# Kernel tuning notes

Hardware: AMD Instinct MI355X
Metric: run time of the kernel (lower is better)

Reference implementation:

```python
import jax, jax.numpy as jnp
import numpy as np


def setup_inputs() -> dict:
    key = jax.random.key(0)
    ks = jax.random.split(key, 13)
    B, W, C = 16, 2048, 512
    inp = {
        "X_sfr": jax.random.normal(ks[0], (B, W, C), dtype=jnp.float32),
        "adj_matrix": jax.random.normal(ks[1], (B, C, C), dtype=jnp.float32),
        "log_temp": jnp.zeros((1,), dtype=jnp.float32),
        "wq": jax.random.normal(ks[2], (1,), dtype=jnp.float32),
        "bq": jax.random.normal(ks[3], (1,), dtype=jnp.float32),
        "wk": jax.random.normal(ks[4], (1,), dtype=jnp.float32),
        "bk": jax.random.normal(ks[5], (1,), dtype=jnp.float32),
        "wv": jax.random.normal(ks[6], (1,), dtype=jnp.float32),
        "bv": jax.random.normal(ks[7], (1,), dtype=jnp.float32),
        "wmu": jax.random.normal(ks[8], (1,), dtype=jnp.float32),
        "bmu": jax.random.normal(ks[9], (1,), dtype=jnp.float32),
        "wsig": jax.random.normal(ks[10], (1,), dtype=jnp.float32),
        "bsig": jax.random.normal(ks[11], (1,), dtype=jnp.float32),
        "k1": 20,
        "k2": 30,
    }
    return inp


def reference(X_sfr, adj_matrix, log_temp, wq, bq, wk, bk, wv, bv, wmu, bmu, wsig, bsig, k1, k2):
    B, W, C = X_sfr.shape
    # spatial propagation: relu + in-degree normalize adjacency
    adj_nonneg = jnp.maximum(adj_matrix, 0.0)
    in_deg = jnp.clip(adj_nonneg.sum(axis=1, keepdims=True), 1e-4)  # [B,1,C]
    adj_norm = adj_nonneg / in_deg
    X_spatial = jnp.einsum('bwi,bij->bwj', X_sfr, adj_norm)  # [B,W,C]

    # static band mask over time: k1 <= |dt| <= k2, fallback to identity rows
    t = jnp.arange(W)
    delta = jnp.abs(t[None, :] - t[:, None])
    band = (delta >= k1) & (delta <= k2)  # [W,W]
    has_valid = band.any(axis=1)
    band = jnp.where(has_valid[:, None], band, jnp.eye(W, dtype=bool))

    # scalar (1->1) q/k/v projections on the temporal token
    temporal_token = X_spatial.mean(axis=2, keepdims=True)  # [B,W,1]
    q = wq * temporal_token + bq                            # [B,W,1]
    k = wk * temporal_token + bk                            # [B,W,1]
    v = wv * X_spatial + bv                                 # [B,W,C]

    temp = jax.nn.softplus(log_temp)[0] + 1e-4
    logits = jnp.matmul(q, jnp.swapaxes(k, 1, 2)) / temp    # [B,W,W] rank-1
    logits = jnp.where(band[None, :, :], logits, -1e9)
    attn = jax.nn.softmax(logits, axis=-1)
    attn = attn * band[None, :, :].astype(attn.dtype)
    attn = attn / (attn.sum(axis=-1, keepdims=True) + 1e-6)

    sacon_scalar = attn.sum(axis=-1, keepdims=True)         # [B,W,1]
    sacon = jnp.broadcast_to(sacon_scalar, (B, W, C))

    X_temporal = jnp.matmul(attn, v)                        # [B,W,C]
    X_fused = X_temporal + X_spatial

    mu = jnp.clip(wmu * X_fused + bmu, -20.0, 20.0)
    sigma_sq = jax.nn.softplus(wsig * X_fused + bsig) + 0.1
    return mu, sigma_sq, sacon
```

## Files before the change

### kernel.cpp

```cpp
#include <hip/hip_runtime.h>
#include <math.h>

#define B_ 16
#define W_ 2048
#define C_ 512

#define OFF_XB    0
#define OFF_BT    33554432
#define OFF_XSP   41943040
#define OFF_TT    75497472

typedef short v8s __attribute__((ext_vector_type(8)));
typedef float v4f __attribute__((ext_vector_type(4)));
typedef float v2f __attribute__((ext_vector_type(2)));
typedef unsigned int u32;

__device__ __forceinline__ float softplusf(float x) {
    return fmaxf(x, 0.f) + log1pf(expf(-fabsf(x)));
}
__device__ __forceinline__ float softplus_fast(float x) {
    return fmaxf(x, 0.f) + __logf(1.f + __expf(-fabsf(x)));
}
__device__ __forceinline__ unsigned short f2bf(float x) {
    unsigned int u = __float_as_uint(x);
    unsigned int r = (u + 0x7FFFu + ((u >> 16) & 1u)) >> 16;
    return (unsigned short)r;
}
__device__ __forceinline__ float bf2f(unsigned int h) {
    return __uint_as_float(h << 16);
}
__device__ __forceinline__ void gload16(const ushort* g, ushort* l) {
    __builtin_amdgcn_global_load_lds(
        (const __attribute__((address_space(1))) u32*)(g),
        (__attribute__((address_space(3))) u32*)(l), 16, 0, 0);
}

__global__ __launch_bounds__(256) void prep_adj(const float* __restrict__ adj,
                                                ushort* __restrict__ Bt) {
    __shared__ float cs[8][32];
    __shared__ float inv[32];
    __shared__ float t[32][33];
    const int b = blockIdx.y, j0 = blockIdx.x * 32;
    const int tx = threadIdx.x & 31, ty = threadIdx.x >> 5;
    const float* src = adj + (size_t)b * C_ * C_;

    float s = 0.f;
#pragma unroll 4
    for (int it = 0; it < C_ / 8; it++)
        s += fmaxf(src[(size_t)(it * 8 + ty) * C_ + j0 + tx], 0.f);
    cs[ty][tx] = s;
    __syncthreads();
    if (ty == 0) {
        float tot = cs[0][tx] + cs[1][tx] + cs[2][tx] + cs[3][tx]
                  + cs[4][tx] + cs[5][tx] + cs[6][tx] + cs[7][tx];
        inv[tx] = 1.f / fmaxf(tot, 1e-4f);
    }

    const int jr = threadIdx.x >> 4;
    const int ic = (threadIdx.x & 15) * 2;
    for (int i0t = 0; i0t < C_; i0t += 32) {
        __syncthreads();
#pragma unroll
        for (int rr = 0; rr < 4; rr++) {
            int ii = ty + rr * 8;
            t[ii][tx] = fmaxf(src[(size_t)(i0t + ii) * C_ + j0 + tx], 0.f);
        }
        __syncthreads();
#pragma unroll
        for (int pp = 0; pp < 2; pp++) {
            int j = jr + pp * 16;
            float iv = inv[j];
            ushort2 o;
            o.x = f2bf(t[ic][j] * iv);
            o.y = f2bf(t[ic + 1][j] * iv);
            *(ushort2*)&Bt[(size_t)b * C_ * C_ + (size_t)(j0 + j) * C_ + i0t + ic] = o;
        }
    }
}

__global__ void convertA(const float* __restrict__ X, ushort* __restrict__ Xb) {
    int idx = blockIdx.x * 256 + threadIdx.x;
    float4 v = ((const float4*)X)[idx];
    ushort4 o;
    o.x = f2bf(v.x); o.y = f2bf(v.y); o.z = f2bf(v.z); o.w = f2bf(v.w);
    ((ushort4*)Xb)[idx] = o;
}

__global__ __launch_bounds__(256) void gemm_mfma(const ushort* __restrict__ Xb,
                                                 const ushort* __restrict__ Bt,
                                                 ushort* __restrict__ Xsp,
                                                 float* __restrict__ tt) {
    __shared__ ushort As[128 * 32];
    __shared__ ushort Bs[128 * 32];
    const int b  = blockIdx.z;
    const int m0 = blockIdx.y * 128;
    const int n0 = blockIdx.x * 128;
    const int tid  = threadIdx.x;
    const int wave = tid >> 6, lane = tid & 63;
    const int quad = lane >> 4, l16 = lane & 15;
    const int mw = (wave & 1) * 64, nw = (wave >> 1) * 64;

    const ushort* Ag = Xb + (size_t)b * W_ * C_ + (size_t)m0 * C_;
    const ushort* Bg = Bt + (size_t)b * C_ * C_ + (size_t)n0 * C_;

    const int sm = tid >> 2;
    const int sk = (tid & 3) * 8;

    v4f acc[4][4];
#pragma unroll
    for (int mt = 0; mt < 4; mt++)
#pragma unroll
        for (int nt = 0; nt < 4; nt++)
            acc[mt][nt] = (v4f){0.f, 0.f, 0.f, 0.f};

    for (int k0 = 0; k0 < C_; k0 += 32) {
        __syncthreads();
        gload16(Ag + (size_t)sm * C_ + k0 + sk,        As + tid * 8);
        gload16(Ag + (size_t)(sm + 64) * C_ + k0 + sk, As + 2048 + tid * 8);
        gload16(Bg + (size_t)sm * C_ + k0 + sk,        Bs + tid * 8);
        gload16(Bg + (size_t)(sm + 64) * C_ + k0 + sk, Bs + 2048 + tid * 8);
        __syncthreads();

        v8s af[4], bf[4];
#pragma unroll
        for (int mt = 0; mt < 4; mt++)
            af[mt] = *(const v8s*)&As[(mw + mt * 16 + l16) * 32 + quad * 8];
#pragma unroll
        for (int nt = 0; nt < 4; nt++)
            bf[nt] = *(const v8s*)&Bs[(nw + nt * 16 + l16) * 32 + quad * 8];
#pragma unroll
        for (int mt = 0; mt < 4; mt++)
#pragma unroll
            for (int nt = 0; nt < 4; nt++)
                acc[mt][nt] = __builtin_amdgcn_mfma_f32_16x16x32_bf16(af[mt], bf[nt], acc[mt][nt], 0, 0, 0);
    }

#pragma unroll
    for (int mt = 0; mt < 4; mt++) {
#pragma unroll
        for (int nt = 0; nt < 4; nt++) {
            int col = n0 + nw + nt * 16 + l16;
#pragma unroll
            for (int r = 0; r < 4; r++) {
                int row = m0 + mw + mt * 16 + quad * 4 + r;
                Xsp[((size_t)b * W_ + row) * C_ + col] = f2bf(acc[mt][nt][r]);
            }
        }
    }

#pragma unroll
    for (int mt = 0; mt < 4; mt++) {
#pragma unroll
        for (int r = 0; r < 4; r++) {
            float s = acc[mt][0][r] + acc[mt][1][r] + acc[mt][2][r] + acc[mt][3][r];
            s += __shfl_xor(s, 1);
            s += __shfl_xor(s, 2);
            s += __shfl_xor(s, 4);
            s += __shfl_xor(s, 8);
            if (l16 == 0) {
                int row = m0 + mw + mt * 16 + quad * 4 + r;
                atomicAdd(&tt[b * W_ + row], s);
            }
        }
    }
}

__global__ __launch_bounds__(256) void final_kernel(const ushort* __restrict__ Xsp,
                                                    const float* __restrict__ tt,
                                                    const float* __restrict__ ltp,
                                                    const float* __restrict__ wqp, const float* __restrict__ bqp,
                                                    const float* __restrict__ wkp, const float* __restrict__ bkp,
                                                    const float* __restrict__ wvp, const float* __restrict__ bvp,
                                                    const float* __restrict__ wmup, const float* __restrict__ bmup,
                                                    const float* __restrict__ wsigp, const float* __restrict__ bsigp,
                                                    const int* __restrict__ k1p, const int* __restrict__ k2p,
                                                    float* __restrict__ out) {
    __shared__ float wlds[4][40][4];
    const int wid = threadIdx.x >> 6, lane = threadIdx.x & 63;
    const int bid = ((int)blockIdx.x & 7) * 256 + ((int)blockIdx.x >> 3);
    const int i0w = bid * 16 + wid * 4;
    const int b = i0w >> 11, ib = i0w & (W_ - 1);
    const int K1 = k1p[0], K2 = k2p[0];
    int ns = K2 - K1 + 1;
    if (ns > 16) ns = 16;
    const int n2 = 2 * ns;
    const int nsL = ns + 3;
    const int nu = 2 * nsL;
    const float Sc = 1.f / (1.f + 1e-6f);

    for (int k = threadIdx.x; k < 4 * 40 * 4; k += 256) ((float*)wlds)[k] = 0.f;
    __syncthreads();

    {
        const float cinv = 1.f / C_;
        const float temp = softplus_fast(ltp[0]) + 1e-4f;
        const float invt = 1.f / temp;
        const float wkc = wkp[0] * cinv, bk = bkp[0];
        const float wqc = wqp[0] * cinv, bq = bqp[0];
        const float* ttb = tt + b * W_;
        const int half = lane >> 5;
        const int s = lane & 31;
#pragma unroll
        for (int rr = 0; rr < 2; rr++) {
            const int r = rr * 2 + half;
            const int i = ib + r;
            const float q = wqc * ttb[i] + bq;
            int j = (s < ns) ? (i - K2 + s) : (i + K1 + (s - ns));
            bool valid = (s < n2) && (j >= 0) && (j < W_);
            int jc = min(max(j, 0), W_ - 1);
            float l = valid ? (q * (wkc * ttb[jc] + bk) * invt) : -1e30f;
            float mx = l;
#pragma unroll
            for (int off = 16; off > 0; off >>= 1) mx = fmaxf(mx, __shfl_xor(mx, off, 32));
            float e = valid ? __expf(l - mx) : 0.f;
            float T = e;
#pragma unroll
            for (int off = 16; off > 0; off >>= 1) T += __shfl_xor(T, off, 32);
            float wsc = (1.f / T) * Sc;
            if (valid) {
                int u = (s < ns) ? (r + s) : (nsL + r + (s - ns));
                wlds[wid][u][r] = e * wsc;
            }
        }
    }
    __syncthreads();

    const ushort* Xbp = Xsp + (size_t)b * W_ * C_;
    const int c8 = lane * 8;
    v2f acc2[4][4];
#pragma unroll
    for (int r = 0; r < 4; r++)
#pragma unroll
        for (int p = 0; p < 4; p++) acc2[r][p] = (v2f){0.f, 0.f};

#pragma unroll 4
    for (int u = 0; u < nu; u++) {
        int j = (u < nsL) ? (ib - K2 + u) : (ib + K1 + (u - nsL));
        j = min(max(j, 0), W_ - 1);
        uint4 v = *(const uint4*)(Xbp + (size_t)j * C_ + c8);
        v2f x[4];
        x[0] = (v2f){bf2f(v.x & 0xffffu), bf2f(v.x >> 16)};
        x[1] = (v2f){bf2f(v.y & 0xffffu), bf2f(v.y >> 16)};
        x[2] = (v2f){bf2f(v.z & 0xffffu), bf2f(v.z >> 16)};
        x[3] = (v2f){bf2f(v.w & 0xffffu), bf2f(v.w >> 16)};
        const v4f w4 = *(const v4f*)&wlds[wid][u][0];
#pragma unroll
        for (int r = 0; r < 4; r++) {
            v2f w2 = (v2f){w4[r], w4[r]};
#pragma unroll
            for (int p = 0; p < 4; p++) acc2[r][p] += w2 * x[p];
        }
    }

    const float wv = wvp[0], bvS = bvp[0] * Sc;
    const float wmu = wmup[0], bmu = bmup[0];
    const float wsig = wsigp[0], bsig = bsigp[0];
    const size_t N = (size_t)B_ * W_ * C_;

#pragma unroll
    for (int r = 0; r < 4; r++) {
        uint4 xv = *(const uint4*)(Xbp + (size_t)(ib + r) * C_ + c8);
        float xs[8];
        xs[0] = bf2f(xv.x & 0xffffu); xs[1] = bf2f(xv.x >> 16);
        xs[2] = bf2f(xv.y & 0xffffu); xs[3] = bf2f(xv.y >> 16);
        xs[4] = bf2f(xv.z & 0xffffu); xs[5] = bf2f(xv.z >> 16);
        xs[6] = bf2f(xv.w & 0xffffu); xs[7] = bf2f(xv.w >> 16);

        float mu[8], sg[8];
#pragma unroll
        for (int k = 0; k < 8; k++) {
            float a = acc2[r][k >> 1][k & 1];
            float xf = fmaf(wv, a, bvS) + xs[k];
            mu[k] = fminf(fmaxf(fmaf(wmu, xf, bmu), -20.f), 20.f);
            sg[k] = softplus_fast(fmaf(wsig, xf, bsig)) + 0.1f;
        }

        const size_t base = (size_t)(i0w + r) * C_ + c8;
        __builtin_nontemporal_store((v4f){mu[0], mu[1], mu[2], mu[3]}, (v4f*)&out[base]);
        __builtin_nontemporal_store((v4f){mu[4], mu[5], mu[6], mu[7]}, (v4f*)&out[base + 4]);
        __builtin_nontemporal_store((v4f){sg[0], sg[1], sg[2], sg[3]}, (v4f*)&out[N + base]);
        __builtin_nontemporal_store((v4f){sg[4], sg[5], sg[6], sg[7]}, (v4f*)&out[N + base + 4]);
        __builtin_nontemporal_store((v4f){Sc, Sc, Sc, Sc}, (v4f*)&out[2 * N + base]);
        __builtin_nontemporal_store((v4f){Sc, Sc, Sc, Sc}, (v4f*)&out[2 * N + base + 4]);
    }
}

extern "C" void kernel_launch(void* const* d_in, const int* in_sizes, int n_in,
                              void* d_out, int out_size, void* d_ws, size_t ws_size,
                              hipStream_t stream) {
    const float* X_sfr = (const float*)d_in[0];
    const float* adj   = (const float*)d_in[1];
    const float* ltp   = (const float*)d_in[2];
    const float* wq    = (const float*)d_in[3];
    const float* bq    = (const float*)d_in[4];
    const float* wk    = (const float*)d_in[5];
    const float* bk    = (const float*)d_in[6];
    const float* wv    = (const float*)d_in[7];
    const float* bv    = (const float*)d_in[8];
    const float* wmu   = (const float*)d_in[9];
    const float* bmu   = (const float*)d_in[10];
    const float* wsig  = (const float*)d_in[11];
    const float* bsig  = (const float*)d_in[12];
    const int*   k1p   = (const int*)d_in[13];
    const int*   k2p   = (const int*)d_in[14];

    char* ws = (char*)d_ws;
    ushort* Xb  = (ushort*)(ws + OFF_XB);
    ushort* Bt  = (ushort*)(ws + OFF_BT);
    ushort* Xsp = (ushort*)(ws + OFF_XSP);
    float*  tt  = (float*)(ws + OFF_TT);
    float*  out = (float*)d_out;

    hipMemsetAsync(tt, 0, B_ * W_ * sizeof(float), stream);

    prep_adj<<<dim3(C_ / 32, B_), 256, 0, stream>>>(adj, Bt);

    convertA<<<(B_ * W_ * C_ / 4) / 256, 256, 0, stream>>>(X_sfr, Xb);

    gemm_mfma<<<dim3(C_ / 128, W_ / 128, B_), 256, 0, stream>>>(Xb, Bt, Xsp, tt);

    final_kernel<<<(B_ * W_) / 16, 256, 0, stream>>>(Xsp, tt, ltp, wq, bq, wk, bk,
                                                     wv, bv, wmu, bmu, wsig, bsig,
                                                     k1p, k2p, out);
}
```

Measured before the change: 408.5 us.

## Split adjacency prep into parallel colsum and tiled transpose; vectorize GEMM epilogue

```diff
diff --git a/kernel.cpp b/kernel.cpp
--- a/kernel.cpp
+++ b/kernel.cpp
@@ -9,15 +9,13 @@
 #define OFF_BT    33554432
 #define OFF_XSP   41943040
 #define OFF_TT    75497472
+#define OFF_CS    75628544
 
 typedef short v8s __attribute__((ext_vector_type(8)));
 typedef float v4f __attribute__((ext_vector_type(4)));
 typedef float v2f __attribute__((ext_vector_type(2)));
 typedef unsigned int u32;
 
-__device__ __forceinline__ float softplusf(float x) {
-    return fmaxf(x, 0.f) + log1pf(expf(-fabsf(x)));
-}
 __device__ __forceinline__ float softplus_fast(float x) {
     return fmaxf(x, 0.f) + __logf(1.f + __expf(-fabsf(x)));
 }
@@ -35,47 +33,61 @@
         (__attribute__((address_space(3))) u32*)(l), 16, 0, 0);
 }
 
-__global__ __launch_bounds__(256) void prep_adj(const float* __restrict__ adj,
-                                                ushort* __restrict__ Bt) {
-    __shared__ float cs[8][32];
-    __shared__ float inv[32];
-    __shared__ float t[32][33];
-    const int b = blockIdx.y, j0 = blockIdx.x * 32;
+__global__ __launch_bounds__(256) void colsum_k(const float* __restrict__ adj,
+                                                float* __restrict__ cs) {
+    __shared__ float red[8][32];
+    const int b = blockIdx.z, j0 = blockIdx.x * 32, r0 = blockIdx.y * 128;
     const int tx = threadIdx.x & 31, ty = threadIdx.x >> 5;
     const float* src = adj + (size_t)b * C_ * C_;
 
     float s = 0.f;
 #pragma unroll 4
-    for (int it = 0; it < C_ / 8; it++)
-        s += fmaxf(src[(size_t)(it * 8 + ty) * C_ + j0 + tx], 0.f);
-    cs[ty][tx] = s;
+    for (int it = 0; it < 16; it++)
+        s += fmaxf(src[(size_t)(r0 + it * 8 + ty) * C_ + j0 + tx], 0.f);
+    red[ty][tx] = s;
     __syncthreads();
     if (ty == 0) {
-        float tot = cs[0][tx] + cs[1][tx] + cs[2][tx] + cs[3][tx]
-                  + cs[4][tx] + cs[5][tx] + cs[6][tx] + cs[7][tx];
-        inv[tx] = 1.f / fmaxf(tot, 1e-4f);
-    }
-
-    const int jr = threadIdx.x >> 4;
-    const int ic = (threadIdx.x & 15) * 2;
-    for (int i0t = 0; i0t < C_; i0t += 32) {
-        __syncthreads();
-#pragma unroll
-        for (int rr = 0; rr < 4; rr++) {
-            int ii = ty + rr * 8;
-            t[ii][tx] = fmaxf(src[(size_t)(i0t + ii) * C_ + j0 + tx], 0.f);
-        }
-        __syncthreads();
-#pragma unroll
-        for (int pp = 0; pp < 2; pp++) {
-            int j = jr + pp * 16;
-            float iv = inv[j];
-            ushort2 o;
-            o.x = f2bf(t[ic][j] * iv);
-            o.y = f2bf(t[ic + 1][j] * iv);
-            *(ushort2*)&Bt[(size_t)b * C_ * C_ + (size_t)(j0 + j) * C_ + i0t + ic] = o;
-        }
-    }
+        float tot = red[0][tx] + red[1][tx] + red[2][tx] + red[3][tx]
+                  + red[4][tx] + red[5][tx] + red[6][tx] + red[7][tx];
+        atomicAdd(&cs[b * C_ + j0 + tx], tot);
+    }
+}
+
+__global__ __launch_bounds__(256) void prep_bt(const float* __restrict__ adj,
+                                               const float* __restrict__ cs,
+                                               ushort* __restrict__ Bt) {
+    __shared__ float t[64][65];
+    __shared__ float invs[64];
+    const int b = blockIdx.z;
+    const int i0 = blockIdx.x * 64;
+    const int j0 = blockIdx.y * 64;
+    const int tid = threadIdx.x;
+    const int tx = tid & 15, ty = tid >> 4;
+
+    if (tid < 64) invs[tid] = 1.f / fmaxf(cs[b * C_ + j0 + tid], 1e-4f);
+
+#pragma unroll
+    for (int p = 0; p < 4; p++) {
+        const int iy = ty + p * 16;
+        const float4 v = *(const float4*)&adj[((size_t)b * C_ + (i0 + iy)) * C_ + j0 + tx * 4];
+        t[iy][tx * 4 + 0] = fmaxf(v.x, 0.f);
+        t[iy][tx * 4 + 1] = fmaxf(v.y, 0.f);
+        t[iy][tx * 4 + 2] = fmaxf(v.z, 0.f);
+        t[iy][tx * 4 + 3] = fmaxf(v.w, 0.f);
+    }
+    __syncthreads();
+
+    const int jj = tid >> 2;
+    const int i4 = (tid & 3) * 16;
+    const float iv = invs[jj];
+    v8s o0, o1;
+#pragma unroll
+    for (int k = 0; k < 8; k++) o0[k] = (short)f2bf(t[i4 + k][jj] * iv);
+#pragma unroll
+    for (int k = 0; k < 8; k++) o1[k] = (short)f2bf(t[i4 + 8 + k][jj] * iv);
+    ushort* dst = &Bt[(size_t)b * C_ * C_ + (size_t)(j0 + jj) * C_ + i0 + i4];
+    *(v8s*)dst       = o0;
+    *(v8s*)(dst + 8) = o1;
 }
 
 __global__ void convertA(const float* __restrict__ X, ushort* __restrict__ Xb) {
@@ -132,36 +144,31 @@
         for (int mt = 0; mt < 4; mt++)
 #pragma unroll
             for (int nt = 0; nt < 4; nt++)
-                acc[mt][nt] = __builtin_amdgcn_mfma_f32_16x16x32_bf16(af[mt], bf[nt], acc[mt][nt], 0, 0, 0);
+                acc[mt][nt] = __builtin_amdgcn_mfma_f32_16x16x32_bf16(bf[nt], af[mt], acc[mt][nt], 0, 0, 0);
     }
 
 #pragma unroll
     for (int mt = 0; mt < 4; mt++) {
+        const int row = m0 + mw + mt * 16 + l16;
+        ushort* rowp = &Xsp[((size_t)b * W_ + row) * C_];
 #pragma unroll
         for (int nt = 0; nt < 4; nt++) {
-            int col = n0 + nw + nt * 16 + l16;
-#pragma unroll
-            for (int r = 0; r < 4; r++) {
-                int row = m0 + mw + mt * 16 + quad * 4 + r;
-                Xsp[((size_t)b * W_ + row) * C_ + col] = f2bf(acc[mt][nt][r]);
-            }
+            const int colb = n0 + nw + nt * 16 + quad * 4;
+            ushort4 o;
+            o.x = f2bf(acc[mt][nt][0]);
+            o.y = f2bf(acc[mt][nt][1]);
+            o.z = f2bf(acc[mt][nt][2]);
+            o.w = f2bf(acc[mt][nt][3]);
+            *(ushort4*)&rowp[colb] = o;
         }
-    }
-
-#pragma unroll
-    for (int mt = 0; mt < 4; mt++) {
-#pragma unroll
-        for (int r = 0; r < 4; r++) {
-            float s = acc[mt][0][r] + acc[mt][1][r] + acc[mt][2][r] + acc[mt][3][r];
-            s += __shfl_xor(s, 1);
-            s += __shfl_xor(s, 2);
-            s += __shfl_xor(s, 4);
-            s += __shfl_xor(s, 8);
-            if (l16 == 0) {
-                int row = m0 + mw + mt * 16 + quad * 4 + r;
-                atomicAdd(&tt[b * W_ + row], s);
-            }
-        }
+        float s = 0.f;
+#pragma unroll
+        for (int nt = 0; nt < 4; nt++)
+#pragma unroll
+            for (int r = 0; r < 4; r++) s += acc[mt][nt][r];
+        s += __shfl_xor(s, 16);
+        s += __shfl_xor(s, 32);
+        if (quad == 0) atomicAdd(&tt[b * W_ + row], s);
     }
 }
 
@@ -309,13 +316,16 @@
     ushort* Bt  = (ushort*)(ws + OFF_BT);
     ushort* Xsp = (ushort*)(ws + OFF_XSP);
     float*  tt  = (float*)(ws + OFF_TT);
+    float*  cs  = (float*)(ws + OFF_CS);
     float*  out = (float*)d_out;
 
-    hipMemsetAsync(tt, 0, B_ * W_ * sizeof(float), stream);
-
-    prep_adj<<<dim3(C_ / 32, B_), 256, 0, stream>>>(adj, Bt);
+    hipMemsetAsync(tt, 0, B_ * W_ * sizeof(float) + B_ * C_ * sizeof(float), stream);
+
+    colsum_k<<<dim3(C_ / 32, 4, B_), 256, 0, stream>>>(adj, cs);
 
     convertA<<<(B_ * W_ * C_ / 4) / 256, 256, 0, stream>>>(X_sfr, Xb);
+
+    prep_bt<<<dim3(C_ / 64, C_ / 64, B_), 256, 0, stream>>>(adj, cs, Bt);
 
     gemm_mfma<<<dim3(C_ / 128, W_ / 128, B_), 256, 0, stream>>>(Xb, Bt, Xsp, tt);
 
```

Measured after the change: 406.4 us. No clear change (-0.5%).
